# Kernel tuning notes

Hardware: AMD Instinct MI355X
Metric: run time of the kernel (lower is better)

The kernel has to match this reference:

```python
import jax, jax.numpy as jnp
import numpy as np

N = 100000
IN_C, HID_C, OUT_C = 256, 128, 2
E = 3200000


def setup_inputs() -> dict:
    key = jax.random.key(0)
    ks = jax.random.split(key, 8)
    x = jax.random.normal(ks[0], (N, IN_C), dtype=jnp.float32)
    edge_index = jax.random.randint(ks[1], (2, E), 0, N, dtype=jnp.int64)
    edge_weight = jax.random.uniform(ks[2], (E,), dtype=jnp.float32)
    # GCNConv params (Glorot-ish init)
    W1 = jax.random.normal(ks[3], (IN_C, HID_C), dtype=jnp.float32) / np.sqrt(IN_C)
    b1 = jnp.zeros((HID_C,), dtype=jnp.float32)
    W2 = jax.random.normal(ks[4], (HID_C, OUT_C), dtype=jnp.float32) / np.sqrt(HID_C)
    b2 = jnp.zeros((OUT_C,), dtype=jnp.float32)
    return {"x": x, "edge_index": edge_index, "edge_weight": edge_weight,
            "W1": W1, "b1": b1, "W2": W2, "b2": b2}


def _gcn_norm(edge_index, edge_weight, num_nodes):
    # Add self-loops with weight 1 (PyG GCNConv default), then symmetric norm.
    loop = jnp.arange(num_nodes, dtype=edge_index.dtype)
    src = jnp.concatenate([edge_index[0], loop])
    dst = jnp.concatenate([edge_index[1], loop])
    w = jnp.concatenate([edge_weight, jnp.ones((num_nodes,), edge_weight.dtype)])
    deg = jax.ops.segment_sum(w, dst, num_segments=num_nodes)
    dinv = jnp.where(deg > 0, jax.lax.rsqrt(deg), 0.0)
    norm = dinv[src] * w * dinv[dst]
    return src, dst, norm


def _gcn_conv(x, src, dst, norm, W, b):
    h = x @ W                                   # [N, C_out] dense transform first
    msg = norm[:, None] * h[src]                # [E+N, C_out] gather + scale
    agg = jax.ops.segment_sum(msg, dst, num_segments=x.shape[0])
    return agg + b


def reference(x, edge_index, edge_weight, W1, b1, W2, b2):
    src, dst, norm = _gcn_norm(edge_index, edge_weight, x.shape[0])
    h = jax.nn.relu(_gcn_conv(x, src, dst, norm, W1, b1))
    # dropout p=0.5 is identity in eval mode
    out = _gcn_conv(h, src, dst, norm, W2, b2)
    return out
```

## Files before the change

### kernel.cpp

```cpp
#include <hip/hip_runtime.h>
#include <hip/hip_fp16.h>

#define IN_C  256
#define HID_C 128
#define OUT_C 2
#define BSH   7
#define NB    128
#define CSH   14
#define MAXNCH 16
#define NKMAX  (MAXNCH * NB)
#define CAP    4608

typedef __attribute__((ext_vector_type(8))) short short8;
typedef __attribute__((ext_vector_type(4))) float float4v;

__device__ __forceinline__ unsigned short f2bf(float f) {
    unsigned u = __float_as_uint(f);
    unsigned r = 0x7fffu + ((u >> 16) & 1u);
    return (unsigned short)((u + r) >> 16);
}
__device__ __forceinline__ unsigned pk2(float a, float b) {
    return (unsigned)f2bf(a) | ((unsigned)f2bf(b) << 16);
}
__device__ __forceinline__ unsigned enc_edge(int src, float w) {
    unsigned h = (unsigned)(__half_as_ushort(__float2half(w)) & 0x7FFF);
    return (h << 17) | (unsigned)src;
}
__device__ __forceinline__ void dec_edge(unsigned rec, int& s, float& w) {
    s = (int)(rec & 0x1FFFFu);
    __half hh;
    *(unsigned short*)&hh = (unsigned short)(rec >> 17);
    w = __half2float(hh);
}
__device__ __forceinline__ float bl(unsigned u) { return __uint_as_float(u << 16); }
__device__ __forceinline__ float bh(unsigned u) { return __uint_as_float(u & 0xffff0000u); }
__device__ __forceinline__ void fma8r(float (&a)[8], uint4 p, float w) {
    a[0] = fmaf(w, bl(p.x), a[0]); a[1] = fmaf(w, bh(p.x), a[1]);
    a[2] = fmaf(w, bl(p.y), a[2]); a[3] = fmaf(w, bh(p.y), a[3]);
    a[4] = fmaf(w, bl(p.z), a[4]); a[5] = fmaf(w, bh(p.z), a[5]);
    a[6] = fmaf(w, bl(p.w), a[6]); a[7] = fmaf(w, bh(p.w), a[7]);
}

__global__ void k_wT(const float* __restrict__ W1, unsigned short* __restrict__ w1t) {
    int i = blockIdx.x * 256 + threadIdx.x;
    if (i >= HID_C * IN_C) return;
    int c = i >> 8, k = i & 255;
    w1t[i] = f2bf(W1[(size_t)k * HID_C + c]);
}

__global__ __launch_bounds__(256) void k_count(const int* __restrict__ ei,
                                               int* __restrict__ gcnt,
                                               int E, int K, int W, int CHv) {
    extern __shared__ int lh[];
    int w = blockIdx.x, t = threadIdx.x;
    for (int b = t; b < K; b += 256) lh[b] = 0;
    __syncthreads();
    int j0 = w * CHv;
    int j1 = min(j0 + CHv, E);
    for (int j = j0 + t; j < j1; j += 256)
        atomicAdd(&lh[ei[E + j] >> BSH], 1);
    __syncthreads();
    for (int b = t; b < K; b += 256) gcnt[(size_t)b * W + w] = lh[b];
}

__global__ __launch_bounds__(256) void k_scanA4(const int* __restrict__ cnt,
                                                int* __restrict__ excl,
                                                int* __restrict__ bsum, int n) {
    __shared__ int ss[256];
    int t = threadIdx.x;
    int base = blockIdx.x * 4096 + t * 16;
    int v[16]; int s = 0;
#pragma unroll
    for (int q = 0; q < 16; q++) { v[q] = (base + q < n) ? cnt[base + q] : 0; s += v[q]; }
    ss[t] = s;
    __syncthreads();
    for (int d = 1; d < 256; d <<= 1) {
        int x = (t >= d) ? ss[t - d] : 0;
        __syncthreads();
        ss[t] += x;
        __syncthreads();
    }
    int pre = (t == 0) ? 0 : ss[t - 1];
    if (t == 255) bsum[blockIdx.x] = ss[255];
    int run = pre;
#pragma unroll
    for (int q = 0; q < 16; q++) { if (base + q < n) excl[base + q] = run; run += v[q]; }
}

__global__ __launch_bounds__(256) void k_scanB(int* __restrict__ bsum, int nb) {
    __shared__ int ss[256];
    int t = threadIdx.x;
    int v[8]; int s = 0;
#pragma unroll
    for (int q = 0; q < 8; q++) {
        int idx = t * 8 + q;
        v[q] = (idx < nb) ? bsum[idx] : 0; s += v[q];
    }
    ss[t] = s;
    __syncthreads();
    for (int d = 1; d < 256; d <<= 1) {
        int x = (t >= d) ? ss[t - d] : 0;
        __syncthreads();
        ss[t] += x;
        __syncthreads();
    }
    int run = (t == 0) ? 0 : ss[t - 1];
#pragma unroll
    for (int q = 0; q < 8; q++) {
        int idx = t * 8 + q;
        if (idx < nb) bsum[idx] = run;
        run += v[q];
    }
}

__global__ __launch_bounds__(256) void k_place(const int* __restrict__ ei,
                                               const float* __restrict__ w,
                                               const int* __restrict__ gpos,
                                               const int* __restrict__ bsum,
                                               int2* __restrict__ ebuf,
                                               int E, int K, int W, int CHv) {
    extern __shared__ int lc[];
    int wg = blockIdx.x, t = threadIdx.x;
    for (int b = t; b < K; b += 256) {
        size_t i = (size_t)b * W + wg;
        lc[b] = gpos[i] + bsum[i >> 12];
    }
    __syncthreads();
    int j0 = wg * CHv;
    int j1 = min(j0 + CHv, E);
    for (int j = j0 + t; j < j1; j += 256) {
        int s = ei[j], d = ei[E + j];
        float wv = w[j];
        int pos = atomicAdd(&lc[d >> BSH], 1);
        ebuf[pos] = make_int2(s | ((d & (NB - 1)) << 17), __float_as_int(wv));
    }
}

__global__ __launch_bounds__(512) void k_sortfine(const int* __restrict__ gcnt,
                                                  const int* __restrict__ bsum,
                                                  const int2* __restrict__ ebuf,
                                                  unsigned* __restrict__ epack2,
                                                  int* __restrict__ rowfine,
                                                  float* __restrict__ dinv,
                                                  int W, int NCH, int E, int K, int N) {
    __shared__ int2 ls[CAP];
    __shared__ unsigned ls2[CAP];
    __shared__ int lh[NKMAX];
    __shared__ int lc[NKMAX];
    __shared__ int ss[512];
    __shared__ float wsum[NB];
    int b = blockIdx.x, t = threadIdx.x;
    size_t i0 = (size_t)b * W;
    int base = gcnt[i0] + bsum[i0 >> 12];
    int next;
    if (b + 1 < K) {
        size_t i1 = (size_t)(b + 1) * W;
        next = gcnt[i1] + bsum[i1 >> 12];
    } else next = E;
    int cnt = next - base;
    int nk = NCH * NB;
    for (int i = t; i < nk; i += 512) lh[i] = 0;
    if (t < NB) wsum[t] = 1.0f;
    __syncthreads();
    bool fits = cnt <= CAP;
    for (int i = t; i < cnt; i += 512) {
        int2 e = ebuf[base + i];
        if (fits) ls[i] = e;
        int src = e.x & 0x1FFFF, dl = (e.x >> 17) & (NB - 1);
        atomicAdd(&lh[(src >> CSH) * NB + dl], 1);
        atomicAdd(&wsum[dl], __int_as_float(e.y));
    }
    __syncthreads();
    {
        int v[4]; int s = 0;
#pragma unroll
        for (int q = 0; q < 4; q++) {
            int idx = t * 4 + q;
            v[q] = (idx < nk) ? lh[idx] : 0; s += v[q];
        }
        ss[t] = s;
        __syncthreads();
        for (int d = 1; d < 512; d <<= 1) {
            int x = (t >= d) ? ss[t - d] : 0;
            __syncthreads();
            ss[t] += x;
            __syncthreads();
        }
        int run = (t == 0) ? 0 : ss[t - 1];
#pragma unroll
        for (int q = 0; q < 4; q++) {
            int idx = t * 4 + q;
            if (idx < nk) lc[idx] = run;
            run += v[q];
        }
    }
    __syncthreads();
    for (int i = t; i < nk; i += 512)
        rowfine[(size_t)b * nk + i] = base + lc[i];
    __syncthreads();
    if (fits) {
        for (int i = t; i < cnt; i += 512) {
            int2 e = ls[i];
            int src = e.x & 0x1FFFF, dl = (e.x >> 17) & (NB - 1);
            int pos = atomicAdd(&lc[(src >> CSH) * NB + dl], 1);
            ls2[pos] = enc_edge(src, __int_as_float(e.y));
        }
        __syncthreads();
        for (int i = t; i < cnt; i += 512)
            epack2[base + i] = ls2[i];
    } else {
        for (int i = t; i < cnt; i += 512) {
            int2 e = ebuf[base + i];
            int src = e.x & 0x1FFFF, dl = (e.x >> 17) & (NB - 1);
            int pos = atomicAdd(&lc[(src >> CSH) * NB + dl], 1);
            epack2[base + pos] = enc_edge(src, __int_as_float(e.y));
        }
    }
    if (t < NB) {
        int node = b * NB + t;
        if (node < N) dinv[node] = rsqrtf(wsum[t]);
    }
    if (b == 0 && t == 0) rowfine[(size_t)K * nk] = E;
}

#define XS_LD 36
__global__ __launch_bounds__(256) void k_gemm1(const float* __restrict__ x,
                                               const unsigned short* __restrict__ w1t,
                                               const float* __restrict__ dinv,
                                               unsigned short* __restrict__ h1b, int n) {
    __shared__ __align__(16) unsigned short xs[64 * XS_LD];
    __shared__ __align__(16) unsigned short ot[64 * 136];
    int tid  = threadIdx.x;
    int row0 = blockIdx.x * 64;
    int wv = tid >> 6, ln = tid & 63;
    int m = ln & 15, quad = ln >> 4;
    float4v acc[8];
#pragma unroll
    for (int ct = 0; ct < 8; ct++) acc[ct] = (float4v){0.f, 0.f, 0.f, 0.f};

    for (int k0 = 0; k0 < IN_C; k0 += 32) {
        __syncthreads();
        {
            int r = tid >> 2, s4 = tid & 3;
            int gr = row0 + r; if (gr >= n) gr = n - 1;
            const float4* px = (const float4*)(x + (size_t)gr * IN_C + k0 + s4 * 8);
            float4 a = px[0], bq = px[1];
            uint2* d = (uint2*)(xs + r * XS_LD + s4 * 8);
            d[0] = make_uint2(pk2(a.x, a.y), pk2(a.z, a.w));
            d[1] = make_uint2(pk2(bq.x, bq.y), pk2(bq.z, bq.w));
        }
        __syncthreads();
        union { uint2 u[2]; short8 v; } af;
        const uint2* pa = (const uint2*)(xs + (wv * 16 + m) * XS_LD + quad * 8);
        af.u[0] = pa[0]; af.u[1] = pa[1];
#pragma unroll
        for (int ct = 0; ct < 8; ct++) {
            union { uint4 u4; short8 v; } bf;
            bf.u4 = *(const uint4*)(w1t + (size_t)(ct * 16 + m) * IN_C + k0 + quad * 8);
            acc[ct] = __builtin_amdgcn_mfma_f32_16x16x32_bf16(af.v, bf.v, acc[ct], 0, 0, 0);
        }
    }
    __syncthreads();
    float4 dv = *(const float4*)(dinv + row0 + wv * 16 + quad * 4);
    const float* dvf = (const float*)&dv;
#pragma unroll
    for (int ct = 0; ct < 8; ct++)
#pragma unroll
        for (int r = 0; r < 4; r++)
            ot[(wv * 16 + quad * 4 + r) * 136 + ct * 16 + m] = f2bf(acc[ct][r] * dvf[r]);
    __syncthreads();
#pragma unroll
    for (int p = 0; p < 4; p++) {
        int idx = p * 256 + tid;
        int r = idx >> 4, c8 = idx & 15;
        if (row0 + r < n)
            *(uint4*)(h1b + (size_t)(row0 + r) * HID_C + c8 * 8) =
                *(const uint4*)(ot + r * 136 + c8 * 8);
    }
}

__global__ __launch_bounds__(512, 4) void k_agg1(const int* __restrict__ rowfine,
                                                 const unsigned* __restrict__ epack2,
                                                 const unsigned short* __restrict__ h1b,
                                                 const float* __restrict__ dinv,
                                                 const float* __restrict__ b1,
                                                 const float* __restrict__ W2,
                                                 float* __restrict__ h2,
                                                 int NCH, int K, int N) {
    int b = blockIdx.x, t = threadIdx.x;
    int wv = t >> 6, lane = t & 63;
    int g = lane >> 4, c16 = lane & 15;
    int nk = NCH * NB;
    const int* rfb = rowfine + (size_t)b * nk;
    const unsigned short* hb = h1b + c16 * 8;
    float au[4][8];
#pragma unroll
    for (int u = 0; u < 4; u++)
#pragma unroll
        for (int k = 0; k < 8; k++) au[u][k] = 0.f;

    for (int ch = 0; ch < NCH; ch++) {
        const int* rf = rfb + ch * NB;
#pragma unroll
        for (int u = 0; u < 4; u++) {
            int d = wv * 16 + u * 4 + g;
            int jb = rf[d], je = rf[d + 1];
            for (int j = jb; j < je; j += 4) {
                int j1 = min(j + 1, je - 1);
                int j2 = min(j + 2, je - 1);
                int j3 = min(j + 3, je - 1);
                unsigned r0 = epack2[j],  r1 = epack2[j1];
                unsigned r2 = epack2[j2], r3 = epack2[j3];
                int s0, s1, s2, s3; float w0, w1, w2, w3;
                dec_edge(r0, s0, w0); dec_edge(r1, s1, w1);
                dec_edge(r2, s2, w2); dec_edge(r3, s3, w3);
                w1 = (j + 1 < je) ? w1 : 0.f;
                w2 = (j + 2 < je) ? w2 : 0.f;
                w3 = (j + 3 < je) ? w3 : 0.f;
                uint4 p0 = *(const uint4*)(hb + ((size_t)s0 << 7));
                uint4 p1 = *(const uint4*)(hb + ((size_t)s1 << 7));
                uint4 p2 = *(const uint4*)(hb + ((size_t)s2 << 7));
                uint4 p3 = *(const uint4*)(hb + ((size_t)s3 << 7));
                fma8r(au[u], p0, w0);
                fma8r(au[u], p1, w1);
                fma8r(au[u], p2, w2);
                fma8r(au[u], p3, w3);
            }
        }
    }
    float4 b1a = *(const float4*)(b1 + c16 * 8);
    float4 b1b = *(const float4*)(b1 + c16 * 8 + 4);
    const float4* wp = (const float4*)(W2 + c16 * 16);
    float4 w0 = wp[0], w1 = wp[1], w2 = wp[2], w3 = wp[3];
#pragma unroll
    for (int u = 0; u < 4; u++) {
        int d = wv * 16 + u * 4 + g;
        int node = b * NB + d;
        bool valid = node < N;
        float di = valid ? dinv[node] : 0.f;
        uint4 sp = make_uint4(0, 0, 0, 0);
        if (valid) sp = *(const uint4*)(h1b + ((size_t)node << 7) + c16 * 8);
        float e0 = fmaxf(fmaf(di, au[u][0] + bl(sp.x), b1a.x), 0.f);
        float e1 = fmaxf(fmaf(di, au[u][1] + bh(sp.x), b1a.y), 0.f);
        float e2 = fmaxf(fmaf(di, au[u][2] + bl(sp.y), b1a.z), 0.f);
        float e3 = fmaxf(fmaf(di, au[u][3] + bh(sp.y), b1a.w), 0.f);
        float e4 = fmaxf(fmaf(di, au[u][4] + bl(sp.z), b1b.x), 0.f);
        float e5 = fmaxf(fmaf(di, au[u][5] + bh(sp.z), b1b.y), 0.f);
        float e6 = fmaxf(fmaf(di, au[u][6] + bl(sp.w), b1b.z), 0.f);
        float e7 = fmaxf(fmaf(di, au[u][7] + bh(sp.w), b1b.w), 0.f);
        float s0 = e0 * w0.x + e1 * w0.z + e2 * w1.x + e3 * w1.z
                 + e4 * w2.x + e5 * w2.z + e6 * w3.x + e7 * w3.z;
        float s1 = e0 * w0.y + e1 * w0.w + e2 * w1.y + e3 * w1.w
                 + e4 * w2.y + e5 * w2.w + e6 * w3.y + e7 * w3.w;
#pragma unroll
        for (int dd = 1; dd < 16; dd <<= 1) {
            s0 += __shfl_xor(s0, dd);
            s1 += __shfl_xor(s1, dd);
        }
        if (c16 == 0 && valid)
            ((float2*)h2)[node] = make_float2(di * s0, di * s1);
    }
}

__global__ __launch_bounds__(256) void k_agg2(const int* __restrict__ rowfine,
                                              const unsigned* __restrict__ epack2,
                                              const float* __restrict__ h2,
                                              const float* __restrict__ dinv,
                                              const float* __restrict__ b2,
                                              float* __restrict__ out,
                                              int NCH, int K, int N) {
    __shared__ float a2[NB * 2];
    int b = blockIdx.x, t = threadIdx.x;
    int d = t & 127, half = t >> 7;
    int nk = NCH * NB;
    const int* rfb = rowfine + (size_t)b * nk;
    float sx = 0.f, sy = 0.f;
    for (int ch = half; ch < NCH; ch += 2) {
        int jb = rfb[ch * NB + d];
        int je = rfb[ch * NB + d + 1];
        for (int j = jb; j < je; j++) {
            unsigned rec = epack2[j];
            int s; float w;
            dec_edge(rec, s, w);
            float2 v = ((const float2*)h2)[s];
            sx = fmaf(w, v.x, sx);
            sy = fmaf(w, v.y, sy);
        }
    }
    if (half == 1) { a2[d * 2] = sx; a2[d * 2 + 1] = sy; }
    __syncthreads();
    if (half == 0) {
        int node = b * NB + d;
        if (node < N) {
            float di = dinv[node];
            float2 hv = ((const float2*)h2)[node];
            sx += a2[d * 2]; sy += a2[d * 2 + 1];
            ((float2*)out)[node] = make_float2(b2[0] + di * (sx + hv.x),
                                               b2[1] + di * (sy + hv.y));
        }
    }
}

static inline size_t algn16(size_t v) { return (v + 15) & ~(size_t)15; }

extern "C" void kernel_launch(void* const* d_in, const int* in_sizes, int n_in,
                              void* d_out, int out_size, void* d_ws, size_t ws_size,
                              hipStream_t stream) {
    const float* x  = (const float*)d_in[0];
    const int*   ei = (const int*)d_in[1];
    const float* ew = (const float*)d_in[2];
    const float* W1 = (const float*)d_in[3];
    const float* b1 = (const float*)d_in[4];
    const float* W2 = (const float*)d_in[5];
    const float* b2 = (const float*)d_in[6];
    float* out = (float*)d_out;

    int N = in_sizes[0] / IN_C;
    int E = in_sizes[2];
    int K = (N + NB - 1) >> BSH;
    int NCH = (N + (1 << CSH) - 1) >> CSH;
    int nk = NCH * NB;
    int W = 256;
    int CHv = (E + W - 1) / W;
    int KW = K * W;

    char* ws = (char*)d_ws;
    float* dinv    = (float*)ws; ws += algn16((size_t)N * 4);
    int*   gcnt    = (int*)ws;   ws += algn16((size_t)KW * 4);
    int*   bsum    = (int*)ws;   ws += 8192;
    int*   rowfine = (int*)ws;   ws += algn16(((size_t)K * nk + 1) * 4);
    unsigned* epack2 = (unsigned*)ws; ws += algn16((size_t)E * 4);
    size_t big = (size_t)E * 8;
    size_t h1sz = (size_t)N * HID_C * 2;
    if (h1sz > big) big = h1sz;
    int2* ebuf = (int2*)ws;
    unsigned short* h1b = (unsigned short*)ws; ws += algn16(big);
    unsigned short* w1t = (unsigned short*)ws; ws += algn16((size_t)HID_C * IN_C * 2);
    float* h2      = (float*)ws; ws += algn16((size_t)N * OUT_C * 4);

    int nb_s4 = (KW + 4095) / 4096;
    size_t lds_k = (size_t)K * 4;

    k_wT      <<<(HID_C * IN_C + 255) / 256, 256, 0, stream>>>(W1, w1t);
    k_count   <<<W, 256, lds_k, stream>>>(ei, gcnt, E, K, W, CHv);
    k_scanA4  <<<nb_s4, 256, 0, stream>>>(gcnt, gcnt, bsum, KW);
    k_scanB   <<<1, 256, 0, stream>>>(bsum, nb_s4);
    k_place   <<<W, 256, lds_k, stream>>>(ei, ew, gcnt, bsum, ebuf, E, K, W, CHv);
    k_sortfine<<<K, 512, 0, stream>>>(gcnt, bsum, ebuf, epack2, rowfine, dinv, W, NCH, E, K, N);
    k_gemm1   <<<(N + 63) / 64, 256, 0, stream>>>(x, w1t, dinv, h1b, N);
    k_agg1    <<<K, 512, 0, stream>>>(rowfine, epack2, h1b, dinv, b1, W2, h2, NCH, K, N);
    k_agg2    <<<K, 256, 0, stream>>>(rowfine, epack2, h2, dinv, b2, out, NCH, K, N);
}
```

Before: 512.8 us.

## Replace two-pass bucket sort with global fine-key histogram, scan and scatter

Builds the CSR-like fine-bucket layout with one global atomic histogram over (dst block, src chunk, dst lane) keys, a global scan, and a direct atomic scatter into epack2. This replaces the per-workgroup count, place into an intermediate buffer, and per-bucket LDS sort. Weighted degree is now accumulated with global float atomics. The gemm now stages W1^T tiles in LDS, and agg1 splits each 128-node block across two workgroups to raise parallelism. The cost is heavy global atomic contention plus a nondeterministic edge order within a bucket.

```diff
diff --git a/kernel.cpp b/kernel.cpp
--- a/kernel.cpp
+++ b/kernel.cpp
@@ -7,9 +7,6 @@
 #define BSH   7
 #define NB    128
 #define CSH   14
-#define MAXNCH 16
-#define NKMAX  (MAXNCH * NB)
-#define CAP    4608
 
 typedef __attribute__((ext_vector_type(8))) short short8;
 typedef __attribute__((ext_vector_type(4))) float float4v;
@@ -41,6 +38,11 @@
     a[6] = fmaf(w, bl(p.w), a[6]); a[7] = fmaf(w, bh(p.w), a[7]);
 }
 
+__global__ void k_zero(int* __restrict__ p, int n) {
+    int i = blockIdx.x * 256 + threadIdx.x;
+    if (i < n) p[i] = 0;
+}
+
 __global__ void k_wT(const float* __restrict__ W1, unsigned short* __restrict__ w1t) {
     int i = blockIdx.x * 256 + threadIdx.x;
     if (i >= HID_C * IN_C) return;
@@ -48,19 +50,19 @@
     w1t[i] = f2bf(W1[(size_t)k * HID_C + c]);
 }
 
-__global__ __launch_bounds__(256) void k_count(const int* __restrict__ ei,
-                                               int* __restrict__ gcnt,
-                                               int E, int K, int W, int CHv) {
-    extern __shared__ int lh[];
-    int w = blockIdx.x, t = threadIdx.x;
-    for (int b = t; b < K; b += 256) lh[b] = 0;
-    __syncthreads();
-    int j0 = w * CHv;
-    int j1 = min(j0 + CHv, E);
-    for (int j = j0 + t; j < j1; j += 256)
-        atomicAdd(&lh[ei[E + j] >> BSH], 1);
-    __syncthreads();
-    for (int b = t; b < K; b += 256) gcnt[(size_t)b * W + w] = lh[b];
+__global__ __launch_bounds__(256) void k_hist(const int* __restrict__ ei,
+                                              const float* __restrict__ ew,
+                                              int* __restrict__ gfine,
+                                              float* __restrict__ wsum,
+                                              int E, int NCH) {
+    int stride = gridDim.x * 256;
+    for (int j = blockIdx.x * 256 + threadIdx.x; j < E; j += stride) {
+        int s = ei[j], d = ei[E + j];
+        float w = ew[j];
+        int key = (d >> BSH) * (NCH << BSH) + ((s >> CSH) << BSH) + (d & (NB - 1));
+        atomicAdd(&gfine[key], 1);
+        atomicAdd(&wsum[d], w);
+    }
 }
 
 __global__ __launch_bounds__(256) void k_scanA4(const int* __restrict__ cnt,
@@ -113,123 +115,46 @@
     }
 }
 
-__global__ __launch_bounds__(256) void k_place(const int* __restrict__ ei,
-                                               const float* __restrict__ w,
-                                               const int* __restrict__ gpos,
-                                               const int* __restrict__ bsum,
-                                               int2* __restrict__ ebuf,
-                                               int E, int K, int W, int CHv) {
-    extern __shared__ int lc[];
-    int wg = blockIdx.x, t = threadIdx.x;
-    for (int b = t; b < K; b += 256) {
-        size_t i = (size_t)b * W + wg;
-        lc[b] = gpos[i] + bsum[i >> 12];
-    }
-    __syncthreads();
-    int j0 = wg * CHv;
-    int j1 = min(j0 + CHv, E);
-    for (int j = j0 + t; j < j1; j += 256) {
+__global__ void k_scanC2(int* __restrict__ gpos, int* __restrict__ cur,
+                         const int* __restrict__ bsum, int n, int E) {
+    int i = blockIdx.x * 256 + threadIdx.x;
+    if (i < n) {
+        int v = gpos[i] + bsum[i >> 12];
+        gpos[i] = v;
+        cur[i] = v;
+    } else if (i == n) {
+        gpos[n] = E;
+    }
+}
+
+__global__ void k_dfin(float* __restrict__ dinv, int N) {
+    int i = blockIdx.x * 256 + threadIdx.x;
+    if (i < N) dinv[i] = rsqrtf(1.0f + dinv[i]);
+}
+
+__global__ __launch_bounds__(256) void k_place2(const int* __restrict__ ei,
+                                                const float* __restrict__ ew,
+                                                int* __restrict__ cur,
+                                                unsigned* __restrict__ epack2,
+                                                int E, int NCH) {
+    int stride = gridDim.x * 256;
+    for (int j = blockIdx.x * 256 + threadIdx.x; j < E; j += stride) {
         int s = ei[j], d = ei[E + j];
-        float wv = w[j];
-        int pos = atomicAdd(&lc[d >> BSH], 1);
-        ebuf[pos] = make_int2(s | ((d & (NB - 1)) << 17), __float_as_int(wv));
-    }
-}
-
-__global__ __launch_bounds__(512) void k_sortfine(const int* __restrict__ gcnt,
-                                                  const int* __restrict__ bsum,
-                                                  const int2* __restrict__ ebuf,
-                                                  unsigned* __restrict__ epack2,
-                                                  int* __restrict__ rowfine,
-                                                  float* __restrict__ dinv,
-                                                  int W, int NCH, int E, int K, int N) {
-    __shared__ int2 ls[CAP];
-    __shared__ unsigned ls2[CAP];
-    __shared__ int lh[NKMAX];
-    __shared__ int lc[NKMAX];
-    __shared__ int ss[512];
-    __shared__ float wsum[NB];
-    int b = blockIdx.x, t = threadIdx.x;
-    size_t i0 = (size_t)b * W;
-    int base = gcnt[i0] + bsum[i0 >> 12];
-    int next;
-    if (b + 1 < K) {
-        size_t i1 = (size_t)(b + 1) * W;
-        next = gcnt[i1] + bsum[i1 >> 12];
-    } else next = E;
-    int cnt = next - base;
-    int nk = NCH * NB;
-    for (int i = t; i < nk; i += 512) lh[i] = 0;
-    if (t < NB) wsum[t] = 1.0f;
-    __syncthreads();
-    bool fits = cnt <= CAP;
-    for (int i = t; i < cnt; i += 512) {
-        int2 e = ebuf[base + i];
-        if (fits) ls[i] = e;
-        int src = e.x & 0x1FFFF, dl = (e.x >> 17) & (NB - 1);
-        atomicAdd(&lh[(src >> CSH) * NB + dl], 1);
-        atomicAdd(&wsum[dl], __int_as_float(e.y));
-    }
-    __syncthreads();
-    {
-        int v[4]; int s = 0;
-#pragma unroll
-        for (int q = 0; q < 4; q++) {
-            int idx = t * 4 + q;
-            v[q] = (idx < nk) ? lh[idx] : 0; s += v[q];
-        }
-        ss[t] = s;
-        __syncthreads();
-        for (int d = 1; d < 512; d <<= 1) {
-            int x = (t >= d) ? ss[t - d] : 0;
-            __syncthreads();
-            ss[t] += x;
-            __syncthreads();
-        }
-        int run = (t == 0) ? 0 : ss[t - 1];
-#pragma unroll
-        for (int q = 0; q < 4; q++) {
-            int idx = t * 4 + q;
-            if (idx < nk) lc[idx] = run;
-            run += v[q];
-        }
-    }
-    __syncthreads();
-    for (int i = t; i < nk; i += 512)
-        rowfine[(size_t)b * nk + i] = base + lc[i];
-    __syncthreads();
-    if (fits) {
-        for (int i = t; i < cnt; i += 512) {
-            int2 e = ls[i];
-            int src = e.x & 0x1FFFF, dl = (e.x >> 17) & (NB - 1);
-            int pos = atomicAdd(&lc[(src >> CSH) * NB + dl], 1);
-            ls2[pos] = enc_edge(src, __int_as_float(e.y));
-        }
-        __syncthreads();
-        for (int i = t; i < cnt; i += 512)
-            epack2[base + i] = ls2[i];
-    } else {
-        for (int i = t; i < cnt; i += 512) {
-            int2 e = ebuf[base + i];
-            int src = e.x & 0x1FFFF, dl = (e.x >> 17) & (NB - 1);
-            int pos = atomicAdd(&lc[(src >> CSH) * NB + dl], 1);
-            epack2[base + pos] = enc_edge(src, __int_as_float(e.y));
-        }
-    }
-    if (t < NB) {
-        int node = b * NB + t;
-        if (node < N) dinv[node] = rsqrtf(wsum[t]);
-    }
-    if (b == 0 && t == 0) rowfine[(size_t)K * nk] = E;
+        float w = ew[j];
+        int key = (d >> BSH) * (NCH << BSH) + ((s >> CSH) << BSH) + (d & (NB - 1));
+        int pos = atomicAdd(&cur[key], 1);
+        epack2[pos] = enc_edge(s, w);
+    }
 }
 
 #define XS_LD 36
+#define WT2_LD 132
 __global__ __launch_bounds__(256) void k_gemm1(const float* __restrict__ x,
                                                const unsigned short* __restrict__ w1t,
                                                const float* __restrict__ dinv,
                                                unsigned short* __restrict__ h1b, int n) {
+    __shared__ __align__(16) unsigned short wt[HID_C * WT2_LD];
     __shared__ __align__(16) unsigned short xs[64 * XS_LD];
-    __shared__ __align__(16) unsigned short ot[64 * 136];
     int tid  = threadIdx.x;
     int row0 = blockIdx.x * 64;
     int wv = tid >> 6, ln = tid & 63;
@@ -238,31 +163,46 @@
 #pragma unroll
     for (int ct = 0; ct < 8; ct++) acc[ct] = (float4v){0.f, 0.f, 0.f, 0.f};
 
-    for (int k0 = 0; k0 < IN_C; k0 += 32) {
-        __syncthreads();
-        {
-            int r = tid >> 2, s4 = tid & 3;
-            int gr = row0 + r; if (gr >= n) gr = n - 1;
-            const float4* px = (const float4*)(x + (size_t)gr * IN_C + k0 + s4 * 8);
-            float4 a = px[0], bq = px[1];
-            uint2* d = (uint2*)(xs + r * XS_LD + s4 * 8);
-            d[0] = make_uint2(pk2(a.x, a.y), pk2(a.z, a.w));
-            d[1] = make_uint2(pk2(bq.x, bq.y), pk2(bq.z, bq.w));
-        }
-        __syncthreads();
-        union { uint2 u[2]; short8 v; } af;
-        const uint2* pa = (const uint2*)(xs + (wv * 16 + m) * XS_LD + quad * 8);
-        af.u[0] = pa[0]; af.u[1] = pa[1];
-#pragma unroll
-        for (int ct = 0; ct < 8; ct++) {
-            union { uint4 u4; short8 v; } bf;
-            bf.u4 = *(const uint4*)(w1t + (size_t)(ct * 16 + m) * IN_C + k0 + quad * 8);
-            acc[ct] = __builtin_amdgcn_mfma_f32_16x16x32_bf16(af.v, bf.v, acc[ct], 0, 0, 0);
+    for (int p = 0; p < 2; p++) {
+        __syncthreads();
+        for (int it = 0; it < 8; it++) {
+            int idx = it * 256 + tid;
+            int c = idx >> 4, kc = idx & 15;
+            const unsigned short* src = w1t + (size_t)c * IN_C + (p << 7) + kc * 8;
+            uint2 a = *(const uint2*)(src);
+            uint2 b = *(const uint2*)(src + 4);
+            *(uint2*)(wt + c * WT2_LD + kc * 8)     = a;
+            *(uint2*)(wt + c * WT2_LD + kc * 8 + 4) = b;
+        }
+        for (int kk = 0; kk < 4; kk++) {
+            int k0 = (p << 7) + kk * 32;
+            __syncthreads();
+            {
+                int r = tid >> 2, s4 = tid & 3;
+                int gr = row0 + r; if (gr >= n) gr = n - 1;
+                const float4* px = (const float4*)(x + (size_t)gr * IN_C + k0 + s4 * 8);
+                float4 a = px[0], bq = px[1];
+                uint2* dxs = (uint2*)(xs + r * XS_LD + s4 * 8);
+                dxs[0] = make_uint2(pk2(a.x, a.y), pk2(a.z, a.w));
+                dxs[1] = make_uint2(pk2(bq.x, bq.y), pk2(bq.z, bq.w));
+            }
+            __syncthreads();
+            union { uint2 u[2]; short8 v; } af;
+            const uint2* pa = (const uint2*)(xs + (wv * 16 + m) * XS_LD + quad * 8);
+            af.u[0] = pa[0]; af.u[1] = pa[1];
+#pragma unroll
+            for (int ct = 0; ct < 8; ct++) {
+                union { uint2 u[2]; short8 v; } bf;
+                const uint2* pb = (const uint2*)(wt + (ct * 16 + m) * WT2_LD + kk * 32 + quad * 8);
+                bf.u[0] = pb[0]; bf.u[1] = pb[1];
+                acc[ct] = __builtin_amdgcn_mfma_f32_16x16x32_bf16(af.v, bf.v, acc[ct], 0, 0, 0);
+            }
         }
     }
     __syncthreads();
     float4 dv = *(const float4*)(dinv + row0 + wv * 16 + quad * 4);
     const float* dvf = (const float*)&dv;
+    unsigned short* ot = wt;
 #pragma unroll
     for (int ct = 0; ct < 8; ct++)
 #pragma unroll
@@ -270,8 +210,8 @@
             ot[(wv * 16 + quad * 4 + r) * 136 + ct * 16 + m] = f2bf(acc[ct][r] * dvf[r]);
     __syncthreads();
 #pragma unroll
-    for (int p = 0; p < 4; p++) {
-        int idx = p * 256 + tid;
+    for (int p4 = 0; p4 < 4; p4++) {
+        int idx = p4 * 256 + tid;
         int r = idx >> 4, c8 = idx & 15;
         if (row0 + r < n)
             *(uint4*)(h1b + (size_t)(row0 + r) * HID_C + c8 * 8) =
@@ -287,23 +227,26 @@
                                                  const float* __restrict__ W2,
                                                  float* __restrict__ h2,
                                                  int NCH, int K, int N) {
-    int b = blockIdx.x, t = threadIdx.x;
+    int blk = blockIdx.x;
+    int b = blk >> 1, half = blk & 1;
+    int t = threadIdx.x;
     int wv = t >> 6, lane = t & 63;
     int g = lane >> 4, c16 = lane & 15;
-    int nk = NCH * NB;
+    int nk = NCH << BSH;
     const int* rfb = rowfine + (size_t)b * nk;
     const unsigned short* hb = h1b + c16 * 8;
-    float au[4][8];
-#pragma unroll
-    for (int u = 0; u < 4; u++)
+    int dbase = (half << 6) + (wv << 3);
+    float au[2][8];
+#pragma unroll
+    for (int u = 0; u < 2; u++)
 #pragma unroll
         for (int k = 0; k < 8; k++) au[u][k] = 0.f;
 
     for (int ch = 0; ch < NCH; ch++) {
-        const int* rf = rfb + ch * NB;
-#pragma unroll
-        for (int u = 0; u < 4; u++) {
-            int d = wv * 16 + u * 4 + g;
+        const int* rf = rfb + (ch << BSH);
+#pragma unroll
+        for (int u = 0; u < 2; u++) {
+            int d = dbase + u * 4 + g;
             int jb = rf[d], je = rf[d + 1];
             for (int j = jb; j < je; j += 4) {
                 int j1 = min(j + 1, je - 1);
@@ -333,9 +276,9 @@
     const float4* wp = (const float4*)(W2 + c16 * 16);
     float4 w0 = wp[0], w1 = wp[1], w2 = wp[2], w3 = wp[3];
 #pragma unroll
-    for (int u = 0; u < 4; u++) {
-        int d = wv * 16 + u * 4 + g;
-        int node = b * NB + d;
+    for (int u = 0; u < 2; u++) {
+        int d = dbase + u * 4 + g;
+        int node = (b << BSH) + d;
         bool valid = node < N;
         float di = valid ? dinv[node] : 0.f;
         uint4 sp = make_uint4(0, 0, 0, 0);
@@ -372,12 +315,12 @@
     __shared__ float a2[NB * 2];
     int b = blockIdx.x, t = threadIdx.x;
     int d = t & 127, half = t >> 7;
-    int nk = NCH * NB;
+    int nk = NCH << BSH;
     const int* rfb = rowfine + (size_t)b * nk;
     float sx = 0.f, sy = 0.f;
     for (int ch = half; ch < NCH; ch += 2) {
-        int jb = rfb[ch * NB + d];
-        int je = rfb[ch * NB + d + 1];
+        int jb = rfb[(ch << BSH) + d];
+        int je = rfb[(ch << BSH) + d + 1];
         for (int j = jb; j < je; j++) {
             unsigned rec = epack2[j];
             int s; float w;
@@ -390,7 +333,7 @@
     if (half == 1) { a2[d * 2] = sx; a2[d * 2 + 1] = sy; }
     __syncthreads();
     if (half == 0) {
-        int node = b * NB + d;
+        int node = (b << BSH) + d;
         if (node < N) {
             float di = dinv[node];
             float2 hv = ((const float2*)h2)[node];
@@ -419,35 +362,31 @@
     int E = in_sizes[2];
     int K = (N + NB - 1) >> BSH;
     int NCH = (N + (1 << CSH) - 1) >> CSH;
-    int nk = NCH * NB;
-    int W = 256;
-    int CHv = (E + W - 1) / W;
-    int KW = K * W;
+    int nk = NCH << BSH;
+    int nf = K * nk;
 
     char* ws = (char*)d_ws;
     float* dinv    = (float*)ws; ws += algn16((size_t)N * 4);
-    int*   gcnt    = (int*)ws;   ws += algn16((size_t)KW * 4);
+    int*   rowfine = (int*)ws;   ws += algn16(((size_t)nf + 1) * 4);
+    int*   cur     = (int*)ws;   ws += algn16((size_t)nf * 4);
     int*   bsum    = (int*)ws;   ws += 8192;
-    int*   rowfine = (int*)ws;   ws += algn16(((size_t)K * nk + 1) * 4);
     unsigned* epack2 = (unsigned*)ws; ws += algn16((size_t)E * 4);
-    size_t big = (size_t)E * 8;
-    size_t h1sz = (size_t)N * HID_C * 2;
-    if (h1sz > big) big = h1sz;
-    int2* ebuf = (int2*)ws;
-    unsigned short* h1b = (unsigned short*)ws; ws += algn16(big);
     unsigned short* w1t = (unsigned short*)ws; ws += algn16((size_t)HID_C * IN_C * 2);
+    unsigned short* h1b = (unsigned short*)ws; ws += algn16((size_t)N * HID_C * 2);
     float* h2      = (float*)ws; ws += algn16((size_t)N * OUT_C * 4);
 
-    int nb_s4 = (KW + 4095) / 4096;
-    size_t lds_k = (size_t)K * 4;
-
-    k_wT      <<<(HID_C * IN_C + 255) / 256, 256, 0, stream>>>(W1, w1t);
-    k_count   <<<W, 256, lds_k, stream>>>(ei, gcnt, E, K, W, CHv);
-    k_scanA4  <<<nb_s4, 256, 0, stream>>>(gcnt, gcnt, bsum, KW);
-    k_scanB   <<<1, 256, 0, stream>>>(bsum, nb_s4);
-    k_place   <<<W, 256, lds_k, stream>>>(ei, ew, gcnt, bsum, ebuf, E, K, W, CHv);
-    k_sortfine<<<K, 512, 0, stream>>>(gcnt, bsum, ebuf, epack2, rowfine, dinv, W, NCH, E, K, N);
-    k_gemm1   <<<(N + 63) / 64, 256, 0, stream>>>(x, w1t, dinv, h1b, N);
-    k_agg1    <<<K, 512, 0, stream>>>(rowfine, epack2, h1b, dinv, b1, W2, h2, NCH, K, N);
-    k_agg2    <<<K, 256, 0, stream>>>(rowfine, epack2, h2, dinv, b2, out, NCH, K, N);
-}
+    int nbf = (nf + 4095) / 4096;
+
+    k_zero  <<<(nf + 1 + 255) / 256, 256, 0, stream>>>(rowfine, nf + 1);
+    k_zero  <<<(N + 255) / 256, 256, 0, stream>>>((int*)dinv, N);
+    k_wT    <<<(HID_C * IN_C + 255) / 256, 256, 0, stream>>>(W1, w1t);
+    k_hist  <<<2048, 256, 0, stream>>>(ei, ew, rowfine, dinv, E, NCH);
+    k_scanA4<<<nbf, 256, 0, stream>>>(rowfine, rowfine, bsum, nf);
+    k_scanB <<<1, 256, 0, stream>>>(bsum, nbf);
+    k_scanC2<<<(nf + 1 + 255) / 256, 256, 0, stream>>>(rowfine, cur, bsum, nf, E);
+    k_dfin  <<<(N + 255) / 256, 256, 0, stream>>>(dinv, N);
+    k_place2<<<2048, 256, 0, stream>>>(ei, ew, cur, epack2, E, NCH);
+    k_gemm1 <<<(N + 63) / 64, 256, 0, stream>>>(x, w1t, dinv, h1b, N);
+    k_agg1  <<<K * 2, 512, 0, stream>>>(rowfine, epack2, h1b, dinv, b1, W2, h2, NCH, K, N);
+    k_agg2  <<<K, 256, 0, stream>>>(rowfine, epack2, h2, dinv, b2, out, NCH, K, N);
+}
```

New measurement: 902.6 us. 1.76x slower.

## Split agg1 blocks in half, stage W1 in LDS, widen count/place grid

Applied to the files above, without the earlier changes.

k_agg1 now launches two blocks per 128-node bucket, each covering 64 destination nodes with fewer accumulators per thread. This doubles grid size and lowers register pressure, at the cost of rereading the rowfine offsets per block. k_gemm1 stages half of the transposed bf16 W1 in shared memory per pass, instead of loading B fragments from global memory for each k-step, and reuses that buffer for the output tile. The count/place grid width W goes from 256 to 512, which enlarges the gcnt prefix arrays. Several multiplies by 128 are also rewritten as shifts.

```diff
diff --git a/kernel.cpp b/kernel.cpp
--- a/kernel.cpp
+++ b/kernel.cpp
@@ -158,7 +158,7 @@
         next = gcnt[i1] + bsum[i1 >> 12];
     } else next = E;
     int cnt = next - base;
-    int nk = NCH * NB;
+    int nk = NCH << BSH;
     for (int i = t; i < nk; i += 512) lh[i] = 0;
     if (t < NB) wsum[t] = 1.0f;
     __syncthreads();
@@ -167,7 +167,7 @@
         int2 e = ebuf[base + i];
         if (fits) ls[i] = e;
         int src = e.x & 0x1FFFF, dl = (e.x >> 17) & (NB - 1);
-        atomicAdd(&lh[(src >> CSH) * NB + dl], 1);
+        atomicAdd(&lh[((src >> CSH) << BSH) + dl], 1);
         atomicAdd(&wsum[dl], __int_as_float(e.y));
     }
     __syncthreads();
@@ -202,7 +202,7 @@
         for (int i = t; i < cnt; i += 512) {
             int2 e = ls[i];
             int src = e.x & 0x1FFFF, dl = (e.x >> 17) & (NB - 1);
-            int pos = atomicAdd(&lc[(src >> CSH) * NB + dl], 1);
+            int pos = atomicAdd(&lc[((src >> CSH) << BSH) + dl], 1);
             ls2[pos] = enc_edge(src, __int_as_float(e.y));
         }
         __syncthreads();
@@ -212,24 +212,25 @@
         for (int i = t; i < cnt; i += 512) {
             int2 e = ebuf[base + i];
             int src = e.x & 0x1FFFF, dl = (e.x >> 17) & (NB - 1);
-            int pos = atomicAdd(&lc[(src >> CSH) * NB + dl], 1);
+            int pos = atomicAdd(&lc[((src >> CSH) << BSH) + dl], 1);
             epack2[base + pos] = enc_edge(src, __int_as_float(e.y));
         }
     }
     if (t < NB) {
-        int node = b * NB + t;
+        int node = (b << BSH) + t;
         if (node < N) dinv[node] = rsqrtf(wsum[t]);
     }
     if (b == 0 && t == 0) rowfine[(size_t)K * nk] = E;
 }
 
 #define XS_LD 36
+#define WT2_LD 132
 __global__ __launch_bounds__(256) void k_gemm1(const float* __restrict__ x,
                                                const unsigned short* __restrict__ w1t,
                                                const float* __restrict__ dinv,
                                                unsigned short* __restrict__ h1b, int n) {
+    __shared__ __align__(16) unsigned short wt[HID_C * WT2_LD];
     __shared__ __align__(16) unsigned short xs[64 * XS_LD];
-    __shared__ __align__(16) unsigned short ot[64 * 136];
     int tid  = threadIdx.x;
     int row0 = blockIdx.x * 64;
     int wv = tid >> 6, ln = tid & 63;
@@ -238,31 +239,46 @@
 #pragma unroll
     for (int ct = 0; ct < 8; ct++) acc[ct] = (float4v){0.f, 0.f, 0.f, 0.f};
 
-    for (int k0 = 0; k0 < IN_C; k0 += 32) {
-        __syncthreads();
-        {
-            int r = tid >> 2, s4 = tid & 3;
-            int gr = row0 + r; if (gr >= n) gr = n - 1;
-            const float4* px = (const float4*)(x + (size_t)gr * IN_C + k0 + s4 * 8);
-            float4 a = px[0], bq = px[1];
-            uint2* d = (uint2*)(xs + r * XS_LD + s4 * 8);
-            d[0] = make_uint2(pk2(a.x, a.y), pk2(a.z, a.w));
-            d[1] = make_uint2(pk2(bq.x, bq.y), pk2(bq.z, bq.w));
-        }
-        __syncthreads();
-        union { uint2 u[2]; short8 v; } af;
-        const uint2* pa = (const uint2*)(xs + (wv * 16 + m) * XS_LD + quad * 8);
-        af.u[0] = pa[0]; af.u[1] = pa[1];
-#pragma unroll
-        for (int ct = 0; ct < 8; ct++) {
-            union { uint4 u4; short8 v; } bf;
-            bf.u4 = *(const uint4*)(w1t + (size_t)(ct * 16 + m) * IN_C + k0 + quad * 8);
-            acc[ct] = __builtin_amdgcn_mfma_f32_16x16x32_bf16(af.v, bf.v, acc[ct], 0, 0, 0);
+    for (int p = 0; p < 2; p++) {
+        __syncthreads();
+        for (int it = 0; it < 8; it++) {
+            int idx = it * 256 + tid;
+            int c = idx >> 4, kc = idx & 15;
+            const unsigned short* src = w1t + (size_t)c * IN_C + (p << 7) + kc * 8;
+            uint2 a = *(const uint2*)(src);
+            uint2 b = *(const uint2*)(src + 4);
+            *(uint2*)(wt + c * WT2_LD + kc * 8)     = a;
+            *(uint2*)(wt + c * WT2_LD + kc * 8 + 4) = b;
+        }
+        for (int kk = 0; kk < 4; kk++) {
+            int k0 = (p << 7) + kk * 32;
+            __syncthreads();
+            {
+                int r = tid >> 2, s4 = tid & 3;
+                int gr = row0 + r; if (gr >= n) gr = n - 1;
+                const float4* px = (const float4*)(x + (size_t)gr * IN_C + k0 + s4 * 8);
+                float4 a = px[0], bq = px[1];
+                uint2* dxs = (uint2*)(xs + r * XS_LD + s4 * 8);
+                dxs[0] = make_uint2(pk2(a.x, a.y), pk2(a.z, a.w));
+                dxs[1] = make_uint2(pk2(bq.x, bq.y), pk2(bq.z, bq.w));
+            }
+            __syncthreads();
+            union { uint2 u[2]; short8 v; } af;
+            const uint2* pa = (const uint2*)(xs + (wv * 16 + m) * XS_LD + quad * 8);
+            af.u[0] = pa[0]; af.u[1] = pa[1];
+#pragma unroll
+            for (int ct = 0; ct < 8; ct++) {
+                union { uint2 u[2]; short8 v; } bf;
+                const uint2* pb = (const uint2*)(wt + (ct * 16 + m) * WT2_LD + kk * 32 + quad * 8);
+                bf.u[0] = pb[0]; bf.u[1] = pb[1];
+                acc[ct] = __builtin_amdgcn_mfma_f32_16x16x32_bf16(af.v, bf.v, acc[ct], 0, 0, 0);
+            }
         }
     }
     __syncthreads();
     float4 dv = *(const float4*)(dinv + row0 + wv * 16 + quad * 4);
     const float* dvf = (const float*)&dv;
+    unsigned short* ot = wt;
 #pragma unroll
     for (int ct = 0; ct < 8; ct++)
 #pragma unroll
@@ -270,8 +286,8 @@
             ot[(wv * 16 + quad * 4 + r) * 136 + ct * 16 + m] = f2bf(acc[ct][r] * dvf[r]);
     __syncthreads();
 #pragma unroll
-    for (int p = 0; p < 4; p++) {
-        int idx = p * 256 + tid;
+    for (int p4 = 0; p4 < 4; p4++) {
+        int idx = p4 * 256 + tid;
         int r = idx >> 4, c8 = idx & 15;
         if (row0 + r < n)
             *(uint4*)(h1b + (size_t)(row0 + r) * HID_C + c8 * 8) =
@@ -287,23 +303,26 @@
                                                  const float* __restrict__ W2,
                                                  float* __restrict__ h2,
                                                  int NCH, int K, int N) {
-    int b = blockIdx.x, t = threadIdx.x;
+    int blk = blockIdx.x;
+    int b = blk >> 1, half = blk & 1;
+    int t = threadIdx.x;
     int wv = t >> 6, lane = t & 63;
     int g = lane >> 4, c16 = lane & 15;
-    int nk = NCH * NB;
+    int nk = NCH << BSH;
     const int* rfb = rowfine + (size_t)b * nk;
     const unsigned short* hb = h1b + c16 * 8;
-    float au[4][8];
-#pragma unroll
-    for (int u = 0; u < 4; u++)
+    int dbase = (half << 6) + (wv << 3);
+    float au[2][8];
+#pragma unroll
+    for (int u = 0; u < 2; u++)
 #pragma unroll
         for (int k = 0; k < 8; k++) au[u][k] = 0.f;
 
     for (int ch = 0; ch < NCH; ch++) {
-        const int* rf = rfb + ch * NB;
-#pragma unroll
-        for (int u = 0; u < 4; u++) {
-            int d = wv * 16 + u * 4 + g;
+        const int* rf = rfb + (ch << BSH);
+#pragma unroll
+        for (int u = 0; u < 2; u++) {
+            int d = dbase + u * 4 + g;
             int jb = rf[d], je = rf[d + 1];
             for (int j = jb; j < je; j += 4) {
                 int j1 = min(j + 1, je - 1);
@@ -333,9 +352,9 @@
     const float4* wp = (const float4*)(W2 + c16 * 16);
     float4 w0 = wp[0], w1 = wp[1], w2 = wp[2], w3 = wp[3];
 #pragma unroll
-    for (int u = 0; u < 4; u++) {
-        int d = wv * 16 + u * 4 + g;
-        int node = b * NB + d;
+    for (int u = 0; u < 2; u++) {
+        int d = dbase + u * 4 + g;
+        int node = (b << BSH) + d;
         bool valid = node < N;
         float di = valid ? dinv[node] : 0.f;
         uint4 sp = make_uint4(0, 0, 0, 0);
@@ -372,12 +391,12 @@
     __shared__ float a2[NB * 2];
     int b = blockIdx.x, t = threadIdx.x;
     int d = t & 127, half = t >> 7;
-    int nk = NCH * NB;
+    int nk = NCH << BSH;
     const int* rfb = rowfine + (size_t)b * nk;
     float sx = 0.f, sy = 0.f;
     for (int ch = half; ch < NCH; ch += 2) {
-        int jb = rfb[ch * NB + d];
-        int je = rfb[ch * NB + d + 1];
+        int jb = rfb[(ch << BSH) + d];
+        int je = rfb[(ch << BSH) + d + 1];
         for (int j = jb; j < je; j++) {
             unsigned rec = epack2[j];
             int s; float w;
@@ -390,7 +409,7 @@
     if (half == 1) { a2[d * 2] = sx; a2[d * 2 + 1] = sy; }
     __syncthreads();
     if (half == 0) {
-        int node = b * NB + d;
+        int node = (b << BSH) + d;
         if (node < N) {
             float di = dinv[node];
             float2 hv = ((const float2*)h2)[node];
@@ -419,8 +438,8 @@
     int E = in_sizes[2];
     int K = (N + NB - 1) >> BSH;
     int NCH = (N + (1 << CSH) - 1) >> CSH;
-    int nk = NCH * NB;
-    int W = 256;
+    int nk = NCH << BSH;
+    int W = 512;
     int CHv = (E + W - 1) / W;
     int KW = K * W;
 
@@ -448,6 +467,6 @@
     k_place   <<<W, 256, lds_k, stream>>>(ei, ew, gcnt, bsum, ebuf, E, K, W, CHv);
     k_sortfine<<<K, 512, 0, stream>>>(gcnt, bsum, ebuf, epack2, rowfine, dinv, W, NCH, E, K, N);
     k_gemm1   <<<(N + 63) / 64, 256, 0, stream>>>(x, w1t, dinv, h1b, N);
-    k_agg1    <<<K, 512, 0, stream>>>(rowfine, epack2, h1b, dinv, b1, W2, h2, NCH, K, N);
+    k_agg1    <<<K * 2, 512, 0, stream>>>(rowfine, epack2, h1b, dinv, b1, W2, h2, NCH, K, N);
     k_agg2    <<<K, 256, 0, stream>>>(rowfine, epack2, h2, dinv, b2, out, NCH, K, N);
 }
```

After: 461.9 us. -9.9%, faster.
